# Optimization experiments

Hardware: AMD Instinct MI355X
Metric: run time of the kernel (lower is better)

The kernel has to match this reference:

```python
import jax, jax.numpy as jnp
import numpy as np

SEQ, BATCH, EMBED = 1024, 2, 768
E = 16            # num_experts = m * N = 2 * 8
FFN_H = 1536      # expert_dim = ceil(3072 / 2)
K_SHARED = 1
K_ROUTE = 3       # (m * top_k) - k_shared = 4 - 1
LN_EPS = 1e-5
NEG_INF = -1e9


def setup_inputs() -> dict:
    key = jax.random.key(0)
    ks = jax.random.split(key, 4)
    x = jax.random.normal(ks[0], (SEQ, BATCH, EMBED), dtype=jnp.float32)
    gate_w = jax.random.normal(ks[1], (EMBED, E), dtype=jnp.float32) * 0.02
    gate_b = jnp.zeros((E,), jnp.float32)
    fc1_w = jax.random.normal(ks[2], (E, EMBED, FFN_H), dtype=jnp.float32) * 0.02
    fc1_b = jnp.zeros((E, FFN_H), jnp.float32)
    ln_w = jnp.ones((E, FFN_H), jnp.float32)
    ln_b = jnp.zeros((E, FFN_H), jnp.float32)
    fc2_w = jax.random.normal(ks[3], (E, FFN_H, EMBED), dtype=jnp.float32) * 0.02
    fc2_b = jnp.zeros((E, EMBED), jnp.float32)
    return {"x": x, "gate_w": gate_w, "gate_b": gate_b,
            "fc1_w": fc1_w, "fc1_b": fc1_b, "ln_w": ln_w, "ln_b": ln_b,
            "fc2_w": fc2_w, "fc2_b": fc2_b}


def reference(x, gate_w, gate_b, fc1_w, fc1_b, ln_w, ln_b, fc2_w, fc2_b):
    S, B, D = x.shape
    T = S * B
    xf = x.reshape(T, D)

    # --- gating: mask shared-expert logits, softmax, top-k over routed probs ---
    scores = xf @ gate_w + gate_b                      # [T, E]
    scores = scores.at[:, :K_SHARED].set(NEG_INF)
    probs = jax.nn.softmax(scores, axis=-1)
    topv, topi = jax.lax.top_k(probs, K_ROUTE)         # [T, K_ROUTE]

    # combine weights: gate prob for selected routed experts, 1.0 for shared experts
    combine = jnp.zeros((T, E), xf.dtype)
    combine = combine.at[jnp.arange(T)[:, None], topi].add(topv)
    combine = combine.at[:, :K_SHARED].add(1.0)        # shared expert(s), weight 1

    # --- per-expert FFN (dense over experts; combine zeros out unselected) ---
    h = jnp.einsum('td,edh->eth', xf, fc1_w) + fc1_b[:, None, :]   # [E, T, H]
    h = jax.nn.gelu(h, approximate=False)              # torch nn.GELU = exact erf
    mu = h.mean(-1, keepdims=True)
    var = h.var(-1, keepdims=True)
    h = (h - mu) * jax.lax.rsqrt(var + LN_EPS) * ln_w[:, None, :] + ln_b[:, None, :]
    y = jnp.einsum('eth,ehd->etd', h, fc2_w) + fc2_b[:, None, :]   # [E, T, D]

    # --- scatter-add combine (gate-weighted sum over experts) ---
    out = jnp.einsum('te,etd->td', combine, y)
    return out.reshape(S, B, D)
```

## Files before the change

kernel.cpp:

```cpp
#include <hip/hip_runtime.h>
#include <cmath>

#define T_TOK 2048
#define D_EMB 768
#define H_FFN 1536
#define NE    16
#define NPAIR (T_TOK * 4)

typedef __attribute__((ext_vector_type(8))) short          short8;
typedef __attribute__((ext_vector_type(8))) unsigned short ushort8;
typedef __attribute__((ext_vector_type(4))) unsigned short ushort4v;
typedef __attribute__((ext_vector_type(4))) float          floatx4;

__device__ __forceinline__ float bf2f(unsigned short u) {
  union { unsigned int i; float f; } v; v.i = ((unsigned int)u) << 16; return v.f;
}
__device__ __forceinline__ unsigned short f2bf(float f) {
  union { float f; unsigned int i; } v; v.f = f;
  unsigned int r = v.i + 0x7fffu + ((v.i >> 16) & 1u);
  return (unsigned short)(r >> 16);
}

__global__ __launch_bounds__(64) void sniff_kernel(
    const unsigned int* __restrict__ x, int* __restrict__ flag)
{
  int lane = threadIdx.x;
  int c = 0;
  for (int i = 0; i < 8; i++) {
    unsigned int w = x[i * 64 + lane];
    unsigned int e = (w >> 7) & 0xFFu;
    c += (e >= 100u && e <= 140u) ? 1 : 0;
  }
  for (int off = 32; off > 0; off >>= 1) c += __shfl_down(c, off);
  if (lane == 0) *flag = (c > 300) ? 1 : 0;
}

__global__ __launch_bounds__(256) void conv_kernel(
    const float* __restrict__ x, const float* __restrict__ fc1b,
    const float* __restrict__ lnw, const float* __restrict__ lnb,
    const float* __restrict__ fc2b,
    unsigned short* __restrict__ dx, unsigned short* __restrict__ dfc1b,
    unsigned short* __restrict__ dlnw, unsigned short* __restrict__ dlnb,
    unsigned short* __restrict__ dfc2b, const int* __restrict__ flag)
{
  if (*flag) return;
  int g = blockIdx.x * 256 + threadIdx.x;
#pragma unroll
  for (int i = 0; i < 3; i++) dx[g + i * 524288] = f2bf(x[g + i * 524288]);
  if (g < 24576) { dfc1b[g] = f2bf(fc1b[g]); dlnw[g] = f2bf(lnw[g]); dlnb[g] = f2bf(lnb[g]); }
  if (g < 12288) dfc2b[g] = f2bf(fc2b[g]);
}

template<int R, int C>
__global__ __launch_bounds__(256) void transpose_kernel(
    const unsigned short* __restrict__ srcB, const float* __restrict__ srcF,
    const int* __restrict__ flag, unsigned short* __restrict__ dst)
{
  __shared__ __align__(16) unsigned short tile[64][72];
  constexpr int RT = R / 64, CT = C / 64;
  int bx  = blockIdx.x;
  int e   = bx / (RT * CT);
  int rem = bx % (RT * CT);
  int rt  = rem / CT, ct = rem % CT;
  int tid = threadIdx.x;
  int r   = tid >> 2;
  int c   = (tid & 3) * 16;
  int xr  = (r & 7) * 8;
  size_t sbase = ((size_t)e * R + rt * 64 + r) * C + ct * 64 + c;
  if (*flag) {
    ushort8 v0 = *(const ushort8*)(srcB + sbase);
    ushort8 v1 = *(const ushort8*)(srcB + sbase + 8);
    *(ushort8*)&tile[r][(c) ^ xr]     = v0;
    *(ushort8*)&tile[r][(c + 8) ^ xr] = v1;
  } else {
    unsigned short tmp[16];
#pragma unroll
    for (int q = 0; q < 4; q++) {
      floatx4 f = *(const floatx4*)(srcF + sbase + q * 4);
#pragma unroll
      for (int j = 0; j < 4; j++) tmp[q * 4 + j] = f2bf(f[j]);
    }
    *(ushort8*)&tile[r][(c) ^ xr]     = *(ushort8*)&tmp[0];
    *(ushort8*)&tile[r][(c + 8) ^ xr] = *(ushort8*)&tmp[8];
  }
  __syncthreads();
  int n  = tid >> 2;
  int k  = (tid & 3) * 16;
  unsigned short outv[16];
#pragma unroll
  for (int j = 0; j < 16; j++) {
    int kr = k + j;
    outv[j] = tile[kr][n ^ ((kr & 7) * 8)];
  }
  size_t dbase = ((size_t)e * C + ct * 64 + n) * R + rt * 64 + k;
  *(ushort8*)(dst + dbase)     = *(ushort8*)&outv[0];
  *(ushort8*)(dst + dbase + 8) = *(ushort8*)&outv[8];
}

__global__ __launch_bounds__(64) void gate_kernel(
    const unsigned short* __restrict__ x16, const float* __restrict__ x32,
    const unsigned short* __restrict__ gw16, const float* __restrict__ gw32,
    const unsigned short* __restrict__ gb16, const float* __restrict__ gb32,
    const int* __restrict__ flag,
    int* __restrict__ psel, float* __restrict__ pw)
{
  int t = blockIdx.x;
  int lane = threadIdx.x;
  int isbf = *flag;
  float acc[NE];
#pragma unroll
  for (int e = 0; e < NE; e++) acc[e] = 0.f;
  if (isbf) {
#pragma unroll
    for (int i = 0; i < D_EMB / 64; i++) {
      int d = i * 64 + lane;
      float xv = bf2f(x16[(size_t)t * D_EMB + d]);
      ushort8 g0 = *(const ushort8*)(gw16 + d * NE);
      ushort8 g1 = *(const ushort8*)(gw16 + d * NE + 8);
#pragma unroll
      for (int e = 0; e < 8; e++) acc[e]     += xv * bf2f(g0[e]);
#pragma unroll
      for (int e = 0; e < 8; e++) acc[8 + e] += xv * bf2f(g1[e]);
    }
  } else {
#pragma unroll
    for (int i = 0; i < D_EMB / 64; i++) {
      int d = i * 64 + lane;
      float xv = x32[(size_t)t * D_EMB + d];
#pragma unroll
      for (int q = 0; q < 4; q++) {
        floatx4 g = *(const floatx4*)(gw32 + d * NE + q * 4);
#pragma unroll
        for (int j = 0; j < 4; j++) acc[q * 4 + j] += xv * g[j];
      }
    }
  }
  __shared__ __align__(16) float sacc[64][NE + 1];
#pragma unroll
  for (int e = 0; e < NE; e++) sacc[lane][e] = acc[e];
  __syncthreads();
  int e = lane & 15, q = lane >> 4;
  float s = 0.f;
#pragma unroll
  for (int i = 0; i < 16; i++) s += sacc[q * 16 + i][e];
  s += __shfl_xor(s, 16);
  s += __shfl_xor(s, 32);
  float sv = s + (isbf ? bf2f(gb16[e]) : gb32[e]);
  if (e == 0) sv = -1e9f;
  float m = sv;
#pragma unroll
  for (int off = 8; off > 0; off >>= 1) m = fmaxf(m, __shfl_xor(m, off));
  float pe = expf(sv - m);
  float den = pe;
#pragma unroll
  for (int off = 8; off > 0; off >>= 1) den += __shfl_xor(den, off);
  float pr = pe / den;
  float val = (e == 0) ? -1.f : pr;
  int sel0, sel1, sel2; float sw0, sw1, sw2;
#pragma unroll
  for (int k = 0; k < 3; k++) {
    float bv = val; int bi = e;
#pragma unroll
    for (int off = 8; off > 0; off >>= 1) {
      float ov = __shfl_xor(bv, off);
      int   oi = __shfl_xor(bi, off);
      if (ov > bv || (ov == bv && oi < bi)) { bv = ov; bi = oi; }
    }
    if (k == 0) { sel0 = bi; sw0 = bv; }
    else if (k == 1) { sel1 = bi; sw1 = bv; }
    else { sel2 = bi; sw2 = bv; }
    if (e == bi) val = -1.f;
  }
  if (lane == 0) {
    psel[t * 4] = 0;    pw[t * 4] = 1.0f;
    psel[t * 4 + 1] = sel0; pw[t * 4 + 1] = sw0;
    psel[t * 4 + 2] = sel1; pw[t * 4 + 2] = sw1;
    psel[t * 4 + 3] = sel2; pw[t * 4 + 3] = sw2;
  }
}

__global__ __launch_bounds__(256) void bucket_kernel(
    const int* __restrict__ psel, int* __restrict__ cnt, int* __restrict__ plist)
{
  int e = blockIdx.x;
  int tid = threadIdx.x;
  int wave = tid >> 6, lane = tid & 63;
  __shared__ int wsum[4];
  __shared__ int base;
  if (tid == 0) base = 0;
  __syncthreads();
  for (int c0 = 0; c0 < NPAIR; c0 += 256) {
    bool mt = (psel[c0 + tid] == e);
    unsigned long long mask = __ballot(mt);
    int wcount = __popcll(mask);
    if (lane == 0) wsum[wave] = wcount;
    __syncthreads();
    int wpre = 0;
#pragma unroll
    for (int w = 0; w < 4; w++) if (w < wave) wpre += wsum[w];
    int total = wsum[0] + wsum[1] + wsum[2] + wsum[3];
    if (mt) {
      int off = __popcll(mask & ((1ULL << lane) - 1ULL));
      plist[e * T_TOK + base + wpre + off] = c0 + tid;
    }
    __syncthreads();
    if (tid == 0) base += total;
    __syncthreads();
  }
  if (tid == 0) cnt[e] = base;
}

template<int KDIM, int NDIM, bool GELU, bool HASBIAS, bool AROWDIV4, bool OUTF32>
__global__ __launch_bounds__(256) void moe_gemm(
    const unsigned short* __restrict__ AO, const unsigned short* __restrict__ AC,
    const unsigned short* __restrict__ BT,
    const unsigned short* __restrict__ biasO, const unsigned short* __restrict__ biasC,
    const int* __restrict__ flag,
    const int* __restrict__ cnt, const int* __restrict__ plist,
    unsigned short* __restrict__ outB, float* __restrict__ outF)
{
  const int NSP = NDIM / 128;
  int bx  = blockIdx.x;
  int e   = bx / (32 * NSP);
  int rem = bx % (32 * NSP);
  int mt  = rem / NSP;
  int ns  = rem % NSP;
  int count = cnt[e];
  if (mt * 64 >= count) return;
  const unsigned short* Abase   = (*flag) ? AO : AC;
  const unsigned short* biasAll = (*flag) ? biasO : biasC;

  __shared__ __align__(16) unsigned short sA[64][72];
  __shared__ __align__(16) unsigned short sB[128][72];
  __shared__ int sp[64];

  int tid = threadIdx.x;
  if (tid < 64) {
    int rg  = mt * 64 + tid;
    int idx = rg < count ? rg : count - 1;
    sp[tid] = plist[e * T_TOK + idx];
  }
  __syncthreads();

  int arow = tid >> 3;
  int ac8  = (tid & 7) * 8;
  int pr0 = sp[arow], pr1 = sp[arow + 32];
  const unsigned short* Aptr0 = Abase + (size_t)(AROWDIV4 ? (pr0 >> 2) : pr0) * KDIM + ac8;
  const unsigned short* Aptr1 = Abase + (size_t)(AROWDIV4 ? (pr1 >> 2) : pr1) * KDIM + ac8;
  int n0 = ns * 128;
  const unsigned short* Bptr =
      BT + ((size_t)e * NDIM + n0 + arow) * KDIM + ac8;

  int lane = tid & 63;
  int wave = tid >> 6;
  int wm   = (wave >> 1) * 32;
  int wn   = (wave & 1) * 64;
  int m16  = lane & 15;
  int quad = lane >> 4;

  floatx4 acc[2][4];
#pragma unroll
  for (int i = 0; i < 2; i++)
#pragma unroll
    for (int j = 0; j < 4; j++) acc[i][j] = (floatx4){0.f, 0.f, 0.f, 0.f};

  ushort8 pa0 = *(const ushort8*)(Aptr0);
  ushort8 pa1 = *(const ushort8*)(Aptr1);
  ushort8 pb0 = *(const ushort8*)(Bptr);
  ushort8 pb1 = *(const ushort8*)(Bptr + (size_t)32 * KDIM);
  ushort8 pb2 = *(const ushort8*)(Bptr + (size_t)64 * KDIM);
  ushort8 pb3 = *(const ushort8*)(Bptr + (size_t)96 * KDIM);

  for (int k0 = 0; k0 < KDIM; k0 += 64) {
    __syncthreads();
    *(ushort8*)&sA[arow][ac8]       = pa0;
    *(ushort8*)&sA[arow + 32][ac8]  = pa1;
    *(ushort8*)&sB[arow][ac8]       = pb0;
    *(ushort8*)&sB[arow + 32][ac8]  = pb1;
    *(ushort8*)&sB[arow + 64][ac8]  = pb2;
    *(ushort8*)&sB[arow + 96][ac8]  = pb3;
    __syncthreads();
    if (k0 + 64 < KDIM) {
      pa0 = *(const ushort8*)(Aptr0 + k0 + 64);
      pa1 = *(const ushort8*)(Aptr1 + k0 + 64);
      pb0 = *(const ushort8*)(Bptr + k0 + 64);
      pb1 = *(const ushort8*)(Bptr + k0 + 64 + (size_t)32 * KDIM);
      pb2 = *(const ushort8*)(Bptr + k0 + 64 + (size_t)64 * KDIM);
      pb3 = *(const ushort8*)(Bptr + k0 + 64 + (size_t)96 * KDIM);
    }
#pragma unroll
    for (int ks = 0; ks < 2; ks++) {
      short8 af0 = *(const short8*)&sA[wm + m16][ks * 32 + quad * 8];
      short8 af1 = *(const short8*)&sA[wm + 16 + m16][ks * 32 + quad * 8];
#pragma unroll
      for (int nt = 0; nt < 4; nt++) {
        short8 bfg = *(const short8*)&sB[wn + nt * 16 + m16][ks * 32 + quad * 8];
        acc[0][nt] = __builtin_amdgcn_mfma_f32_16x16x32_bf16(af0, bfg, acc[0][nt], 0, 0, 0);
        acc[1][nt] = __builtin_amdgcn_mfma_f32_16x16x32_bf16(af1, bfg, acc[1][nt], 0, 0, 0);
      }
    }
  }
#pragma unroll
  for (int sub = 0; sub < 2; sub++) {
#pragma unroll
    for (int nt = 0; nt < 4; nt++) {
#pragma unroll
      for (int r = 0; r < 4; r++) {
        int row_local = wm + sub * 16 + quad * 4 + r;
        int rg = mt * 64 + row_local;
        if (rg < count) {
          int col = n0 + wn + nt * 16 + m16;
          float v = acc[sub][nt][r];
          if (HASBIAS) v += bf2f(biasAll[e * NDIM + col]);
          if (GELU)    v = 0.5f * v * (1.f + erff(v * 0.70710678118654752f));
          int p = sp[row_local];
          if (OUTF32) outF[(size_t)p * NDIM + col] = v;
          else        outB[(size_t)p * NDIM + col] = f2bf(v);
        }
      }
    }
  }
}

__global__ __launch_bounds__(256) void ln_kernel(
    unsigned short* __restrict__ Hbuf,
    const unsigned short* __restrict__ lnwO, const unsigned short* __restrict__ lnwC,
    const unsigned short* __restrict__ lnbO, const unsigned short* __restrict__ lnbC,
    const int* __restrict__ psel, const float* __restrict__ pw,
    const int* __restrict__ flag)
{
  int p = blockIdx.x;
  int tid = threadIdx.x;
  int e = psel[p];
  int isbf = *flag;
  const unsigned short* lnw = isbf ? lnwO : lnwC;
  const unsigned short* lnb = isbf ? lnbO : lnbC;
  unsigned short* hr = Hbuf + (size_t)p * H_FFN;
  bool act = tid < 192;
  float v[8];
  float s = 0.f, sq = 0.f;
  if (act) {
    ushort8 hv = *(const ushort8*)(hr + tid * 8);
#pragma unroll
    for (int j = 0; j < 8; j++) { v[j] = bf2f(hv[j]); s += v[j]; sq += v[j] * v[j]; }
  }
#pragma unroll
  for (int off = 32; off > 0; off >>= 1) {
    s  += __shfl_down(s, off);
    sq += __shfl_down(sq, off);
  }
  __shared__ float red[8];
  int wave = tid >> 6, lane = tid & 63;
  if (lane == 0) { red[wave * 2] = s; red[wave * 2 + 1] = sq; }
  __syncthreads();
  __shared__ float mv[2];
  if (tid == 0) {
    float S = 0.f, Q = 0.f;
    for (int w = 0; w < 4; w++) { S += red[w * 2]; Q += red[w * 2 + 1]; }
    float mu  = S * (1.f / H_FFN);
    float var = Q * (1.f / H_FFN) - mu * mu;
    mv[0] = mu; mv[1] = rsqrtf(var + 1e-5f);
  }
  __syncthreads();
  if (act) {
    float mu = mv[0], rstd = mv[1];
    float w = pw[p];
    ushort8 lw = *(const ushort8*)(lnw + e * H_FFN + tid * 8);
    ushort8 lb = *(const ushort8*)(lnb + e * H_FFN + tid * 8);
    ushort8 o;
#pragma unroll
    for (int j = 0; j < 8; j++)
      o[j] = f2bf(((v[j] - mu) * rstd * bf2f(lw[j]) + bf2f(lb[j])) * w);
    *(ushort8*)(hr + tid * 8) = o;
  }
}

__global__ __launch_bounds__(256) void combine_kernel(
    const float* __restrict__ Y,
    const unsigned short* __restrict__ b2O, const unsigned short* __restrict__ b2C,
    const int* __restrict__ psel, const float* __restrict__ pw,
    unsigned short* __restrict__ out16, float* __restrict__ out32,
    const int* __restrict__ flag)
{
  int t = blockIdx.x;
  int tid = threadIdx.x;
  if (tid >= 192) return;
  int isbf = *flag;
  const unsigned short* b2 = isbf ? b2O : b2C;
  int e1 = psel[t * 4 + 1], e2 = psel[t * 4 + 2], e3 = psel[t * 4 + 3];
  float w1 = pw[t * 4 + 1], w2 = pw[t * 4 + 2], w3 = pw[t * 4 + 3];
  int d = tid * 4;
  const float* Yb = Y + (size_t)t * 4 * D_EMB + d;
  floatx4 y0 = *(const floatx4*)(Yb);
  floatx4 y1 = *(const floatx4*)(Yb + D_EMB);
  floatx4 y2 = *(const floatx4*)(Yb + 2 * D_EMB);
  floatx4 y3 = *(const floatx4*)(Yb + 3 * D_EMB);
  ushort4v b0 = *(const ushort4v*)(b2 + d);
  ushort4v bb1 = *(const ushort4v*)(b2 + e1 * D_EMB + d);
  ushort4v bb2 = *(const ushort4v*)(b2 + e2 * D_EMB + d);
  ushort4v bb3 = *(const ushort4v*)(b2 + e3 * D_EMB + d);
  if (isbf) {
    ushort4v o;
#pragma unroll
    for (int j = 0; j < 4; j++) {
      float a = y0[j] + y1[j] + y2[j] + y3[j] + bf2f(b0[j])
              + w1 * bf2f(bb1[j]) + w2 * bf2f(bb2[j]) + w3 * bf2f(bb3[j]);
      o[j] = f2bf(a);
    }
    *(ushort4v*)(out16 + (size_t)t * D_EMB + d) = o;
  } else {
    floatx4 o;
#pragma unroll
    for (int j = 0; j < 4; j++)
      o[j] = y0[j] + y1[j] + y2[j] + y3[j] + bf2f(b0[j])
           + w1 * bf2f(bb1[j]) + w2 * bf2f(bb2[j]) + w3 * bf2f(bb3[j]);
    *(floatx4*)(out32 + (size_t)t * D_EMB + d) = o;
  }
}

extern "C" void kernel_launch(void* const* d_in, const int* in_sizes, int n_in,
                              void* d_out, int out_size, void* d_ws, size_t ws_size,
                              hipStream_t stream)
{
  (void)in_sizes; (void)n_in; (void)out_size; (void)ws_size;
  char* ws = (char*)d_ws;
  int*   cnt   = (int*)ws;
  int*   plist = (int*)(ws + 256);
  int*   psel  = (int*)(ws + 131328);
  float* pw    = (float*)(ws + 164096);
  int*   flag  = (int*)(ws + 196864);
  unsigned short* fc1bC = (unsigned short*)(ws + 197120);
  unsigned short* lnwC  = (unsigned short*)(ws + 246272);
  unsigned short* lnbC  = (unsigned short*)(ws + 295424);
  unsigned short* fc2bC = (unsigned short*)(ws + 344576);
  unsigned short* xC    = (unsigned short*)(ws + 524288);
  unsigned short* Hbuf  = (unsigned short*)(ws + 3670016);
  float*          Ybuf  = (float*)(ws + 28835840);
  unsigned short* fc1T  = (unsigned short*)(ws + 54001664);
  unsigned short* fc2T  = (unsigned short*)(ws + 91750400);

  sniff_kernel<<<1, 64, 0, stream>>>((const unsigned int*)d_in[0], flag);

  conv_kernel<<<2048, 256, 0, stream>>>(
      (const float*)d_in[0], (const float*)d_in[4], (const float*)d_in[5],
      (const float*)d_in[6], (const float*)d_in[8],
      xC, fc1bC, lnwC, lnbC, fc2bC, flag);

  transpose_kernel<768, 1536><<<16 * 12 * 24, 256, 0, stream>>>(
      (const unsigned short*)d_in[3], (const float*)d_in[3], flag, fc1T);
  transpose_kernel<1536, 768><<<16 * 24 * 12, 256, 0, stream>>>(
      (const unsigned short*)d_in[7], (const float*)d_in[7], flag, fc2T);

  gate_kernel<<<T_TOK, 64, 0, stream>>>(
      (const unsigned short*)d_in[0], (const float*)d_in[0],
      (const unsigned short*)d_in[1], (const float*)d_in[1],
      (const unsigned short*)d_in[2], (const float*)d_in[2],
      flag, psel, pw);

  bucket_kernel<<<NE, 256, 0, stream>>>(psel, cnt, plist);

  moe_gemm<D_EMB, H_FFN, true, true, true, false>
      <<<NE * 32 * (H_FFN / 128), 256, 0, stream>>>(
      (const unsigned short*)d_in[0], xC, fc1T,
      (const unsigned short*)d_in[4], fc1bC,
      flag, cnt, plist, Hbuf, nullptr);

  ln_kernel<<<NPAIR, 256, 0, stream>>>(
      Hbuf,
      (const unsigned short*)d_in[5], lnwC,
      (const unsigned short*)d_in[6], lnbC,
      psel, pw, flag);

  moe_gemm<H_FFN, D_EMB, false, false, false, true>
      <<<NE * 32 * (D_EMB / 128), 256, 0, stream>>>(
      Hbuf, Hbuf, fc2T,
      nullptr, nullptr,
      flag, cnt, plist, nullptr, Ybuf);

  combine_kernel<<<T_TOK, 256, 0, stream>>>(
      Ybuf,
      (const unsigned short*)d_in[8], fc2bC,
      psel, pw,
      (unsigned short*)d_out, (float*)d_out, flag);
}
```

Before: 368.1 us.

## Enlarge MoE GEMM M-tile to 128 rows and reorder block mapping

After: 385.9 us. +4.8%, slower.

```diff
diff --git a/kernel.cpp b/kernel.cpp
--- a/kernel.cpp
+++ b/kernel.cpp
@@ -220,97 +220,100 @@
     unsigned short* __restrict__ outB, float* __restrict__ outF)
 {
   const int NSP = NDIM / 128;
-  int bx  = blockIdx.x;
-  int e   = bx / (32 * NSP);
-  int rem = bx % (32 * NSP);
-  int mt  = rem / NSP;
-  int ns  = rem % NSP;
+  int bx = blockIdx.x;
+  int s  = bx % (NE * NSP);
+  int mt = bx / (NE * NSP);
+  int e  = s / NSP;
+  int ns = s % NSP;
   int count = cnt[e];
-  if (mt * 64 >= count) return;
+  if (mt * 128 >= count) return;
   const unsigned short* Abase   = (*flag) ? AO : AC;
   const unsigned short* biasAll = (*flag) ? biasO : biasC;
 
-  __shared__ __align__(16) unsigned short sA[64][72];
+  __shared__ __align__(16) unsigned short sA[128][72];
   __shared__ __align__(16) unsigned short sB[128][72];
-  __shared__ int sp[64];
+  __shared__ int sp[128];
 
   int tid = threadIdx.x;
-  if (tid < 64) {
-    int rg  = mt * 64 + tid;
+  if (tid < 128) {
+    int rg  = mt * 128 + tid;
     int idx = rg < count ? rg : count - 1;
     sp[tid] = plist[e * T_TOK + idx];
   }
   __syncthreads();
 
-  int arow = tid >> 3;
-  int ac8  = (tid & 7) * 8;
-  int pr0 = sp[arow], pr1 = sp[arow + 32];
-  const unsigned short* Aptr0 = Abase + (size_t)(AROWDIV4 ? (pr0 >> 2) : pr0) * KDIM + ac8;
-  const unsigned short* Aptr1 = Abase + (size_t)(AROWDIV4 ? (pr1 >> 2) : pr1) * KDIM + ac8;
-  int n0 = ns * 128;
-  const unsigned short* Bptr =
-      BT + ((size_t)e * NDIM + n0 + arow) * KDIM + ac8;
+  int n0   = ns * 128;
+  int r_st = tid >> 3;
+  int k8   = (tid & 7) * 8;
+  const unsigned short* Ap[4];
+  const unsigned short* Bp[4];
+#pragma unroll
+  for (int i = 0; i < 4; i++) {
+    int row = r_st + 32 * i;
+    int p   = sp[row];
+    Ap[i] = Abase + (size_t)(AROWDIV4 ? (p >> 2) : p) * KDIM + k8;
+    Bp[i] = BT + ((size_t)e * NDIM + n0 + row) * KDIM + k8;
+  }
 
   int lane = tid & 63;
   int wave = tid >> 6;
-  int wm   = (wave >> 1) * 32;
+  int wm   = (wave >> 1) * 64;
   int wn   = (wave & 1) * 64;
   int m16  = lane & 15;
   int quad = lane >> 4;
 
-  floatx4 acc[2][4];
-#pragma unroll
-  for (int i = 0; i < 2; i++)
+  floatx4 acc[4][4];
+#pragma unroll
+  for (int i = 0; i < 4; i++)
 #pragma unroll
     for (int j = 0; j < 4; j++) acc[i][j] = (floatx4){0.f, 0.f, 0.f, 0.f};
 
-  ushort8 pa0 = *(const ushort8*)(Aptr0);
-  ushort8 pa1 = *(const ushort8*)(Aptr1);
-  ushort8 pb0 = *(const ushort8*)(Bptr);
-  ushort8 pb1 = *(const ushort8*)(Bptr + (size_t)32 * KDIM);
-  ushort8 pb2 = *(const ushort8*)(Bptr + (size_t)64 * KDIM);
-  ushort8 pb3 = *(const ushort8*)(Bptr + (size_t)96 * KDIM);
+  ushort8 pa[4], pb[4];
+#pragma unroll
+  for (int i = 0; i < 4; i++) { pa[i] = *(const ushort8*)(Ap[i]); pb[i] = *(const ushort8*)(Bp[i]); }
 
   for (int k0 = 0; k0 < KDIM; k0 += 64) {
     __syncthreads();
-    *(ushort8*)&sA[arow][ac8]       = pa0;
-    *(ushort8*)&sA[arow + 32][ac8]  = pa1;
-    *(ushort8*)&sB[arow][ac8]       = pb0;
-    *(ushort8*)&sB[arow + 32][ac8]  = pb1;
-    *(ushort8*)&sB[arow + 64][ac8]  = pb2;
-    *(ushort8*)&sB[arow + 96][ac8]  = pb3;
+#pragma unroll
+    for (int i = 0; i < 4; i++) {
+      *(ushort8*)&sA[r_st + 32 * i][k8] = pa[i];
+      *(ushort8*)&sB[r_st + 32 * i][k8] = pb[i];
+    }
     __syncthreads();
     if (k0 + 64 < KDIM) {
-      pa0 = *(const ushort8*)(Aptr0 + k0 + 64);
-      pa1 = *(const ushort8*)(Aptr1 + k0 + 64);
-      pb0 = *(const ushort8*)(Bptr + k0 + 64);
-      pb1 = *(const ushort8*)(Bptr + k0 + 64 + (size_t)32 * KDIM);
-      pb2 = *(const ushort8*)(Bptr + k0 + 64 + (size_t)64 * KDIM);
-      pb3 = *(const ushort8*)(Bptr + k0 + 64 + (size_t)96 * KDIM);
+#pragma unroll
+      for (int i = 0; i < 4; i++) {
+        pa[i] = *(const ushort8*)(Ap[i] + k0 + 64);
+        pb[i] = *(const ushort8*)(Bp[i] + k0 + 64);
+      }
     }
 #pragma unroll
     for (int ks = 0; ks < 2; ks++) {
-      short8 af0 = *(const short8*)&sA[wm + m16][ks * 32 + quad * 8];
-      short8 af1 = *(const short8*)&sA[wm + 16 + m16][ks * 32 + quad * 8];
-#pragma unroll
-      for (int nt = 0; nt < 4; nt++) {
-        short8 bfg = *(const short8*)&sB[wn + nt * 16 + m16][ks * 32 + quad * 8];
-        acc[0][nt] = __builtin_amdgcn_mfma_f32_16x16x32_bf16(af0, bfg, acc[0][nt], 0, 0, 0);
-        acc[1][nt] = __builtin_amdgcn_mfma_f32_16x16x32_bf16(af1, bfg, acc[1][nt], 0, 0, 0);
-      }
-    }
-  }
-#pragma unroll
-  for (int sub = 0; sub < 2; sub++) {
-#pragma unroll
-    for (int nt = 0; nt < 4; nt++) {
+      short8 af[4], bf[4];
+#pragma unroll
+      for (int mi = 0; mi < 4; mi++)
+        af[mi] = *(const short8*)&sA[wm + mi * 16 + m16][ks * 32 + quad * 8];
+#pragma unroll
+      for (int ni = 0; ni < 4; ni++)
+        bf[ni] = *(const short8*)&sB[wn + ni * 16 + m16][ks * 32 + quad * 8];
+#pragma unroll
+      for (int mi = 0; mi < 4; mi++)
+#pragma unroll
+        for (int ni = 0; ni < 4; ni++)
+          acc[mi][ni] = __builtin_amdgcn_mfma_f32_16x16x32_bf16(af[mi], bf[ni], acc[mi][ni], 0, 0, 0);
+    }
+  }
+#pragma unroll
+  for (int mi = 0; mi < 4; mi++) {
+#pragma unroll
+    for (int ni = 0; ni < 4; ni++) {
 #pragma unroll
       for (int r = 0; r < 4; r++) {
-        int row_local = wm + sub * 16 + quad * 4 + r;
-        int rg = mt * 64 + row_local;
+        int row_local = wm + mi * 16 + quad * 4 + r;
+        int rg = mt * 128 + row_local;
         if (rg < count) {
-          int col = n0 + wn + nt * 16 + m16;
-          float v = acc[sub][nt][r];
+          int col = n0 + wn + ni * 16 + m16;
+          float v = acc[mi][ni][r];
           if (HASBIAS) v += bf2f(biasAll[e * NDIM + col]);
           if (GELU)    v = 0.5f * v * (1.f + erff(v * 0.70710678118654752f));
           int p = sp[row_local];
@@ -322,7 +325,7 @@
   }
 }
 
-__global__ __launch_bounds__(256) void ln_kernel(
+__global__ __launch_bounds__(192) void ln_kernel(
     unsigned short* __restrict__ Hbuf,
     const unsigned short* __restrict__ lnwO, const unsigned short* __restrict__ lnwC,
     const unsigned short* __restrict__ lnbO, const unsigned short* __restrict__ lnbC,
@@ -336,46 +339,41 @@
   const unsigned short* lnw = isbf ? lnwO : lnwC;
   const unsigned short* lnb = isbf ? lnbO : lnbC;
   unsigned short* hr = Hbuf + (size_t)p * H_FFN;
-  bool act = tid < 192;
   float v[8];
   float s = 0.f, sq = 0.f;
-  if (act) {
-    ushort8 hv = *(const ushort8*)(hr + tid * 8);
-#pragma unroll
-    for (int j = 0; j < 8; j++) { v[j] = bf2f(hv[j]); s += v[j]; sq += v[j] * v[j]; }
-  }
+  ushort8 hv = *(const ushort8*)(hr + tid * 8);
+#pragma unroll
+  for (int j = 0; j < 8; j++) { v[j] = bf2f(hv[j]); s += v[j]; sq += v[j] * v[j]; }
 #pragma unroll
   for (int off = 32; off > 0; off >>= 1) {
     s  += __shfl_down(s, off);
     sq += __shfl_down(sq, off);
   }
-  __shared__ float red[8];
+  __shared__ float red[6];
   int wave = tid >> 6, lane = tid & 63;
   if (lane == 0) { red[wave * 2] = s; red[wave * 2 + 1] = sq; }
   __syncthreads();
   __shared__ float mv[2];
   if (tid == 0) {
     float S = 0.f, Q = 0.f;
-    for (int w = 0; w < 4; w++) { S += red[w * 2]; Q += red[w * 2 + 1]; }
+    for (int w = 0; w < 3; w++) { S += red[w * 2]; Q += red[w * 2 + 1]; }
     float mu  = S * (1.f / H_FFN);
     float var = Q * (1.f / H_FFN) - mu * mu;
     mv[0] = mu; mv[1] = rsqrtf(var + 1e-5f);
   }
   __syncthreads();
-  if (act) {
-    float mu = mv[0], rstd = mv[1];
-    float w = pw[p];
-    ushort8 lw = *(const ushort8*)(lnw + e * H_FFN + tid * 8);
-    ushort8 lb = *(const ushort8*)(lnb + e * H_FFN + tid * 8);
-    ushort8 o;
-#pragma unroll
-    for (int j = 0; j < 8; j++)
-      o[j] = f2bf(((v[j] - mu) * rstd * bf2f(lw[j]) + bf2f(lb[j])) * w);
-    *(ushort8*)(hr + tid * 8) = o;
-  }
-}
-
-__global__ __launch_bounds__(256) void combine_kernel(
+  float mu = mv[0], rstd = mv[1];
+  float w = pw[p];
+  ushort8 lw = *(const ushort8*)(lnw + e * H_FFN + tid * 8);
+  ushort8 lb = *(const ushort8*)(lnb + e * H_FFN + tid * 8);
+  ushort8 o;
+#pragma unroll
+  for (int j = 0; j < 8; j++)
+    o[j] = f2bf(((v[j] - mu) * rstd * bf2f(lw[j]) + bf2f(lb[j])) * w);
+  *(ushort8*)(hr + tid * 8) = o;
+}
+
+__global__ __launch_bounds__(192) void combine_kernel(
     const float* __restrict__ Y,
     const unsigned short* __restrict__ b2O, const unsigned short* __restrict__ b2C,
     const int* __restrict__ psel, const float* __restrict__ pw,
@@ -384,7 +382,6 @@
 {
   int t = blockIdx.x;
   int tid = threadIdx.x;
-  if (tid >= 192) return;
   int isbf = *flag;
   const unsigned short* b2 = isbf ? b2O : b2C;
   int e1 = psel[t * 4 + 1], e2 = psel[t * 4 + 2], e3 = psel[t * 4 + 3];
@@ -460,24 +457,24 @@
   bucket_kernel<<<NE, 256, 0, stream>>>(psel, cnt, plist);
 
   moe_gemm<D_EMB, H_FFN, true, true, true, false>
-      <<<NE * 32 * (H_FFN / 128), 256, 0, stream>>>(
+      <<<16 * NE * (H_FFN / 128), 256, 0, stream>>>(
       (const unsigned short*)d_in[0], xC, fc1T,
       (const unsigned short*)d_in[4], fc1bC,
       flag, cnt, plist, Hbuf, nullptr);
 
-  ln_kernel<<<NPAIR, 256, 0, stream>>>(
+  ln_kernel<<<NPAIR, 192, 0, stream>>>(
       Hbuf,
       (const unsigned short*)d_in[5], lnwC,
       (const unsigned short*)d_in[6], lnbC,
       psel, pw, flag);
 
   moe_gemm<H_FFN, D_EMB, false, false, false, true>
-      <<<NE * 32 * (D_EMB / 128), 256, 0, stream>>>(
+      <<<16 * NE * (D_EMB / 128), 256, 0, stream>>>(
       Hbuf, Hbuf, fc2T,
       nullptr, nullptr,
       flag, cnt, plist, nullptr, Ybuf);
 
-  combine_kernel<<<T_TOK, 256, 0, stream>>>(
+  combine_kernel<<<T_TOK, 192, 0, stream>>>(
       Ybuf,
       (const unsigned short*)d_in[8], fc2bC,
       psel, pw,
```
